# Optimization experiments

Measured on AMD Instinct MI355X. Metric: run time of the kernel, lower is better.

## Reference

```python
import jax, jax.numpy as jnp
import numpy as np

N = 100000      # nodes
E = 1600000     # edges
D = 128         # hidden_dim
H = 8           # num_heads
DH = D // H     # per-head dim (out_dim in MultiHeadAttentionLayer)
EPS = 1e-5


def layer_norm(x, g, b):
    mu = jnp.mean(x, axis=-1, keepdims=True)
    var = jnp.var(x, axis=-1, keepdims=True)
    return (x - mu) * jax.lax.rsqrt(var + EPS) * g + b


def setup_inputs() -> dict:
    key = jax.random.key(0)
    ks = jax.random.split(key, 16)
    s = 1.0 / np.sqrt(D)
    inp = {
        "h": jax.random.normal(ks[0], (N, D), jnp.float32),
        "src": jax.random.randint(ks[1], (E,), 0, N, jnp.int32),
        "dst": jax.random.randint(ks[2], (E,), 0, N, jnp.int32),
        # attention projections (use_bias=False)
        "Wq": jax.random.uniform(ks[3], (D, D), jnp.float32, -s, s),
        "Wk": jax.random.uniform(ks[4], (D, D), jnp.float32, -s, s),
        "Wv": jax.random.uniform(ks[5], (D, D), jnp.float32, -s, s),
        # output projection O (bias=True)
        "Wo": jax.random.uniform(ks[6], (D, D), jnp.float32, -s, s),
        "bo": jnp.zeros((D,), jnp.float32),
        # layer norms
        "g1": jnp.ones((D,), jnp.float32),
        "b1": jnp.zeros((D,), jnp.float32),
        "g2": jnp.ones((D,), jnp.float32),
        "b2": jnp.zeros((D,), jnp.float32),
        # FFN
        "W1": jax.random.uniform(ks[7], (D, 2 * D), jnp.float32, -s, s),
        "c1": jnp.zeros((2 * D,), jnp.float32),
        "W2": jax.random.uniform(ks[8], (2 * D, D), jnp.float32, -1.0 / np.sqrt(2 * D), 1.0 / np.sqrt(2 * D)),
        "c2": jnp.zeros((D,), jnp.float32),
    }
    return inp


def reference(h, src, dst, Wq, Wk, Wv, Wo, bo, g1, b1, g2, b2, W1, c1, W2, c2):
    n = h.shape[0]
    Q = (h @ Wq).reshape(n, H, DH)
    K = (h @ Wk).reshape(n, H, DH)
    V = (h @ Wv).reshape(n, H, DH)

    # per-edge score: (K[src] * Q[dst]).sum(-1), scaled exp with clamp
    score = jnp.einsum('ehd,ehd->eh', K[src], Q[dst])          # [E, H]
    score = jnp.exp(jnp.clip(score / np.sqrt(DH), -5.0, 5.0))  # [E, H]

    # scatter-sum aggregation into destination nodes
    wV = jax.ops.segment_sum(V[src] * score[:, :, None], dst, num_segments=n)  # [N, H, DH]
    z = jax.ops.segment_sum(score, dst, num_segments=n)                        # [N, H]

    # possible_empty=True: divide only where z > 0
    zb = z[:, :, None]
    head_out = jnp.where(zb > 0, wV / jnp.where(zb > 0, zb, 1.0), wV)

    a = head_out.reshape(n, D) @ Wo + bo
    hh = layer_norm(h + a, g1, b1)
    ff = jax.nn.relu(hh @ W1 + c1) @ W2 + c2
    return layer_norm(hh + ff, g2, b2)
```

## Files before the change

### kernel.cpp

```cpp
#include <hip/hip_runtime.h>
#include <hip/hip_bf16.h>

#define D 128

typedef __attribute__((ext_vector_type(8))) short short8;
typedef __attribute__((ext_vector_type(4))) float float4v;
typedef __attribute__((ext_vector_type(2))) float float2v;

__device__ __forceinline__ float4v mfma16(short8 a, short8 b, float4v c) {
  return __builtin_amdgcn_mfma_f32_16x16x32_bf16(a, b, c, 0, 0, 0);
}
__device__ __forceinline__ float b2f(__hip_bfloat16 x) { return __bfloat162float(x); }
__device__ __forceinline__ __hip_bfloat16 f2b(float x) { return __float2bfloat16(x); }
__device__ __forceinline__ unsigned short f2b_bits(float x) {
  __hip_bfloat16 h = __float2bfloat16(x);
  return *reinterpret_cast<unsigned short*>(&h);
}

__device__ __forceinline__ float ldf(const float* p, size_t i) { return p[i]; }
__device__ __forceinline__ float ldf(const __hip_bfloat16* p, size_t i) { return b2f(p[i]); }
__device__ __forceinline__ void stf(float* p, size_t i, float v) { p[i] = v; }
__device__ __forceinline__ void stf(__hip_bfloat16* p, size_t i, float v) { p[i] = f2b(v); }

__device__ __forceinline__ void unpack2(unsigned w, float& lo, float& hi) {
  lo = __uint_as_float(w << 16);
  hi = __uint_as_float(w & 0xffff0000u);
}
__device__ __forceinline__ float2v up2(unsigned w) {
  float2v r;
  r.x = __uint_as_float(w << 16);
  r.y = __uint_as_float(w & 0xffff0000u);
  return r;
}
__device__ __forceinline__ unsigned char f2fp8(float x) {
  int r = __builtin_amdgcn_cvt_pk_fp8_f32(x, x, 0, false);
  return (unsigned char)(r & 0xff);
}
__device__ __forceinline__ float2v cvt2lo(unsigned w) {
  return __builtin_amdgcn_cvt_pk_f32_fp8(w, false);
}
__device__ __forceinline__ float2v cvt2hi(unsigned w) {
  return __builtin_amdgcn_cvt_pk_f32_fp8(w, true);
}

__global__ void k_cast_w(const float* __restrict__ wq, const float* __restrict__ wk,
                         const float* __restrict__ wv, const float* __restrict__ wo,
                         const float* __restrict__ w1, const float* __restrict__ w2,
                         __hip_bfloat16* __restrict__ oq, __hip_bfloat16* __restrict__ ok,
                         __hip_bfloat16* __restrict__ ov, __hip_bfloat16* __restrict__ oo,
                         __hip_bfloat16* __restrict__ o1, __hip_bfloat16* __restrict__ o2) {
  int i = blockIdx.x * 256 + threadIdx.x;
  if (i < 49152) {
    int m = i & 16383;
    const float* s = (i < 16384) ? wq : (i < 32768) ? wk : wv;
    __hip_bfloat16* o = (i < 16384) ? oq : (i < 32768) ? ok : ov;
    int j = m & 7, t = m >> 3;
    int col = t & 127, cq = t >> 7;
    int row = (cq >> 2) * 32 + (cq & 3) * 8 + j;
    o[m] = f2b(s[row * 128 + col]);
  }
  else if (i < 65536) oo[i - 49152] = f2b(wo[i - 49152]);
  else if (i < 98304) o1[i - 65536] = f2b(w1[i - 65536]);
  else o2[i - 98304] = f2b(w2[i - 98304]);
}

#define MAXB 512

__global__ void k_bhist(const int* __restrict__ dst, int* __restrict__ bh, int E) {
  __shared__ int cnt[MAXB];
  for (int i = threadIdx.x; i < MAXB; i += 256) cnt[i] = 0;
  __syncthreads();
  for (int e = blockIdx.x * 256 + threadIdx.x; e < E; e += gridDim.x * 256)
    atomicAdd(&cnt[dst[e] >> 8], 1);
  __syncthreads();
  for (int i = threadIdx.x; i < MAXB; i += 256)
    if (cnt[i]) atomicAdd(&bh[i], cnt[i]);
}

__global__ void k_bscan(const int* __restrict__ bh, int* __restrict__ bbase,
                        int* __restrict__ bcur, int B) {
  __shared__ int sd[MAXB];
  int t = threadIdx.x;
  int v = (t < B) ? bh[t] : 0;
  sd[t] = v;
  __syncthreads();
  for (int o = 1; o < MAXB; o <<= 1) {
    int x = (t >= o) ? sd[t - o] : 0;
    __syncthreads();
    sd[t] += x;
    __syncthreads();
  }
  if (t < B) {
    int e = sd[t] - v;
    bbase[t] = e;
    bcur[t] = e;
  }
}

__global__ __launch_bounds__(256) void k_bin(const int* __restrict__ src,
                                             const int* __restrict__ dst,
                                             int* __restrict__ bcur,
                                             uint2* __restrict__ binned, int E) {
  __shared__ int cnt[MAXB];
  __shared__ int base[MAXB];
  const int t = threadIdx.x;
  const int e0 = blockIdx.x * 4096;
  for (int i = t; i < MAXB; i += 256) cnt[i] = 0;
  __syncthreads();
  int myb[16], myr[16], ms[16], md[16];
#pragma unroll
  for (int j = 0; j < 16; ++j) {
    int e = e0 + j * 256 + t;
    if (e < E) {
      int d = dst[e];
      ms[j] = src[e];
      md[j] = d;
      int b = d >> 8;
      myb[j] = b;
      myr[j] = atomicAdd(&cnt[b], 1);
    } else {
      myb[j] = -1;
    }
  }
  __syncthreads();
  for (int i = t; i < MAXB; i += 256)
    base[i] = cnt[i] ? atomicAdd(&bcur[i], cnt[i]) : 0;
  __syncthreads();
#pragma unroll
  for (int j = 0; j < 16; ++j)
    if (myb[j] >= 0)
      binned[(size_t)base[myb[j]] + myr[j]] = make_uint2((unsigned)ms[j], (unsigned)md[j]);
}

__global__ __launch_bounds__(256) void k_fine(const uint2* __restrict__ binned,
                                              const int* __restrict__ bh,
                                              const int* __restrict__ bbase,
                                              int* __restrict__ deg,
                                              int* __restrict__ offs,
                                              int* __restrict__ csr, int N) {
  __shared__ int cnt[256];
  __shared__ int cur[256];
  __shared__ int sd[256];
  const int b = blockIdx.x, t = threadIdx.x;
  const int node0 = b << 8;
  cnt[t] = 0;
  __syncthreads();
  const int s0 = bbase[b], len = bh[b];
  for (int i = t; i < len; i += 256) atomicAdd(&cnt[binned[(size_t)s0 + i].y & 255], 1);
  __syncthreads();
  int v = cnt[t];
  sd[t] = v;
  __syncthreads();
  for (int o = 1; o < 256; o <<= 1) {
    int x = (t >= o) ? sd[t - o] : 0;
    __syncthreads();
    sd[t] += x;
    __syncthreads();
  }
  int excl = sd[t] - v;
  cur[t] = excl;
  int node = node0 + t;
  if (node < N) {
    deg[node] = v;
    offs[node] = s0 + excl;
  }
  __syncthreads();
  for (int i = t; i < len; i += 256) {
    uint2 ed = binned[(size_t)s0 + i];
    int p = atomicAdd(&cur[ed.y & 255], 1);
    csr[s0 + p] = (int)ed.x;
  }
}

__global__ __launch_bounds__(512, 2) void gemm_qkv2(const float* __restrict__ A,
                                                    const short8* __restrict__ BqF,
                                                    const short8* __restrict__ BkF,
                                                    const short8* __restrict__ BvF,
                                                    __hip_bfloat16* __restrict__ Q,
                                                    unsigned char* __restrict__ KV8,
                                                    int Nrow) {
  const int t = threadIdx.x;
  const int lane = t & 63;
  const int ct = t >> 6;
  const int n = lane & 15, quad = lane >> 4;
  short8 fq[4], fk[4], fv[4];
#pragma unroll
  for (int c = 0; c < 4; ++c) {
    int fi = (c * 4 + quad) * 128 + ct * 16 + n;
    fq[c] = BqF[fi];
    fk[c] = BkF[fi];
    fv[c] = BvF[fi];
  }
  int ntiles = Nrow >> 4;
  const int koff = ct * 32 + ((n >> 3) << 4) + (n & 7);
  for (int rt = blockIdx.x; rt < ntiles; rt += gridDim.x) {
    float4v aq = {0.f, 0.f, 0.f, 0.f}, ak = aq, av = aq;
    const float* Ap = A + (size_t)(rt * 16 + n) * 128 + quad * 8;
#pragma unroll
    for (int c = 0; c < 4; ++c) {
      float4 u0 = *(const float4*)(Ap + c * 32);
      float4 u1 = *(const float4*)(Ap + c * 32 + 4);
      short8 a;
      a[0] = (short)f2b_bits(u0.x); a[1] = (short)f2b_bits(u0.y);
      a[2] = (short)f2b_bits(u0.z); a[3] = (short)f2b_bits(u0.w);
      a[4] = (short)f2b_bits(u1.x); a[5] = (short)f2b_bits(u1.y);
      a[6] = (short)f2b_bits(u1.z); a[7] = (short)f2b_bits(u1.w);
      aq = mfma16(a, fq[c], aq);
      ak = mfma16(a, fk[c], ak);
      av = mfma16(a, fv[c], av);
    }
#pragma unroll
    for (int r = 0; r < 4; ++r) {
      int grow = rt * 16 + quad * 4 + r;
      Q[(size_t)grow * 128 + ct * 16 + n] = f2b(aq[r]);
      size_t b = (size_t)grow * 256 + koff;
      KV8[b] = f2fp8(ak[r]);
      KV8[b + 8] = f2fp8(av[r]);
    }
  }
}

template <int K, typename TR, typename TO>
__global__ __launch_bounds__(512) void ln_gemm(const short* __restrict__ A,
                                               const short* __restrict__ B,
                                               const float* __restrict__ bias,
                                               const TR* __restrict__ resid,
                                               const float* __restrict__ gam,
                                               const float* __restrict__ bet,
                                               TO* __restrict__ Out, int Nrow) {
  __shared__ float tile[2][16][132];
  const int t = threadIdx.x;
  const int lane = t & 63;
  const int ct = t >> 6;
  const int n = lane & 15, quad = lane >> 4;
  short8 bfr[K / 32];
#pragma unroll
  for (int c = 0; c < K / 32; ++c) {
    short8 tmp;
#pragma unroll
    for (int j = 0; j < 8; ++j)
      tmp[j] = B[(size_t)(c * 32 + quad * 8 + j) * 128 + ct * 16 + n];
    bfr[c] = tmp;
  }
  float biasv = bias[ct * 16 + n];
  const int row2 = t >> 5, sub = t & 31;
  float ga0 = gam[sub],      ga1 = gam[sub + 32];
  float ga2 = gam[sub + 64], ga3 = gam[sub + 96];
  float be0 = bet[sub],      be1 = bet[sub + 32];
  float be2 = bet[sub + 64], be3 = bet[sub + 96];
  int ntiles = Nrow >> 4;
  int pp = 0;
  for (int rt = blockIdx.x; rt < ntiles; rt += gridDim.x, pp ^= 1) {
    float4v acc = {0.f, 0.f, 0.f, 0.f};
    const short* Ap = A + (size_t)(rt * 16 + n) * K + quad * 8;
#pragma unroll
    for (int c = 0; c < K / 32; ++c)
      acc = mfma16(*(const short8*)(Ap + c * 32), bfr[c], acc);
#pragma unroll
    for (int r = 0; r < 4; ++r) {
      int rr = quad * 4 + r;
      size_t g = (size_t)(rt * 16 + rr) * 128 + ct * 16 + n;
      tile[pp][rr][ct * 16 + n] = acc[r] + biasv + ldf(resid, g);
    }
    __syncthreads();
    float x0 = tile[pp][row2][sub], x1 = tile[pp][row2][sub + 32];
    float x2 = tile[pp][row2][sub + 64], x3 = tile[pp][row2][sub + 96];
    float s = x0 + x1 + x2 + x3;
    float s2 = x0 * x0 + x1 * x1 + x2 * x2 + x3 * x3;
#pragma unroll
    for (int o = 16; o >= 1; o >>= 1) {
      s += __shfl_xor(s, o);
      s2 += __shfl_xor(s2, o);
    }
    float mean = s * 0.0078125f;
    float var = s2 * 0.0078125f - mean * mean;
    float rstd = rsqrtf(var + 1e-5f);
    size_t base = (size_t)(rt * 16 + row2) * 128;
    stf(Out, base + sub,      (x0 - mean) * rstd * ga0 + be0);
    stf(Out, base + sub + 32, (x1 - mean) * rstd * ga1 + be1);
    stf(Out, base + sub + 64, (x2 - mean) * rstd * ga2 + be2);
    stf(Out, base + sub + 96, (x3 - mean) * rstd * ga3 + be3);
  }
}

__global__ __launch_bounds__(512) void ffn_ln(const short* __restrict__ hh,
                                              const short* __restrict__ W1b,
                                              const float* __restrict__ c1,
                                              const short* __restrict__ W2b,
                                              const float* __restrict__ c2,
                                              const float* __restrict__ gam,
                                              const float* __restrict__ bet,
                                              float* __restrict__ Out, int Nrow) {
  __shared__ short mid[16][264];
  __shared__ float tile[16][132];
  const int t = threadIdx.x;
  const int lane = t & 63;
  const int wv = t >> 6;
  const int n = lane & 15, quad = lane >> 4;
  short8 f1[2][4];
  float b1v[2];
#pragma unroll
  for (int cc = 0; cc < 2; ++cc) {
    int col = (wv * 2 + cc) * 16 + n;
#pragma unroll
    for (int c = 0; c < 4; ++c) {
      short8 tmp;
#pragma unroll
      for (int j = 0; j < 8; ++j)
        tmp[j] = W1b[(size_t)(c * 32 + quad * 8 + j) * 256 + col];
      f1[cc][c] = tmp;
    }
    b1v[cc] = c1[col];
  }
  short8 f2[8];
#pragma unroll
  for (int c = 0; c < 8; ++c) {
    short8 tmp;
#pragma unroll
    for (int j = 0; j < 8; ++j)
      tmp[j] = W2b[(size_t)(c * 32 + quad * 8 + j) * 128 + wv * 16 + n];
    f2[c] = tmp;
  }
  float b2v = c2[wv * 16 + n];
  const int row2 = t >> 5, sub = t & 31;
  float ga0 = gam[sub],      ga1 = gam[sub + 32];
  float ga2 = gam[sub + 64], ga3 = gam[sub + 96];
  float be0 = bet[sub],      be1 = bet[sub + 32];
  float be2 = bet[sub + 64], be3 = bet[sub + 96];
  int ntiles = Nrow >> 4;
  for (int rt = blockIdx.x; rt < ntiles; rt += gridDim.x) {
    float4v a1[2];
    a1[0] = (float4v){0.f, 0.f, 0.f, 0.f};
    a1[1] = a1[0];
    const short* Ap = hh + (size_t)(rt * 16 + n) * 128 + quad * 8;
#pragma unroll
    for (int c = 0; c < 4; ++c) {
      short8 a = *(const short8*)(Ap + c * 32);
      a1[0] = mfma16(a, f1[0][c], a1[0]);
      a1[1] = mfma16(a, f1[1][c], a1[1]);
    }
#pragma unroll
    for (int cc = 0; cc < 2; ++cc)
#pragma unroll
      for (int r = 0; r < 4; ++r)
        mid[quad * 4 + r][(wv * 2 + cc) * 16 + n] =
            (short)f2b_bits(fmaxf(a1[cc][r] + b1v[cc], 0.f));
    __syncthreads();
    float4v acc = {0.f, 0.f, 0.f, 0.f};
#pragma unroll
    for (int c = 0; c < 8; ++c) {
      short8 a = *(const short8*)&mid[n][quad * 8 + c * 32];
      acc = mfma16(a, f2[c], acc);
    }
#pragma unroll
    for (int r = 0; r < 4; ++r) {
      int rr = quad * 4 + r;
      size_t g = (size_t)(rt * 16 + rr) * 128 + wv * 16 + n;
      tile[rr][wv * 16 + n] = acc[r] + b2v + b2f(((const __hip_bfloat16*)hh)[g]);
    }
    __syncthreads();
    float x0 = tile[row2][sub], x1 = tile[row2][sub + 32];
    float x2 = tile[row2][sub + 64], x3 = tile[row2][sub + 96];
    float s = x0 + x1 + x2 + x3;
    float s2 = x0 * x0 + x1 * x1 + x2 * x2 + x3 * x3;
#pragma unroll
    for (int o = 16; o >= 1; o >>= 1) {
      s += __shfl_xor(s, o);
      s2 += __shfl_xor(s2, o);
    }
    float mean = s * 0.0078125f;
    float var = s2 * 0.0078125f - mean * mean;
    float rstd = rsqrtf(var + 1e-5f);
    size_t base = (size_t)(rt * 16 + row2) * 128;
    Out[base + sub]      = (x0 - mean) * rstd * ga0 + be0;
    Out[base + sub + 32] = (x1 - mean) * rstd * ga1 + be1;
    Out[base + sub + 64] = (x2 - mean) * rstd * ga2 + be2;
    Out[base + sub + 96] = (x3 - mean) * rstd * ga3 + be3;
  }
}

__global__ __launch_bounds__(256) void attn_agg5(const uint4* __restrict__ Q4,
                                                 const uint4* __restrict__ KV8,
                                                 const int* __restrict__ offs,
                                                 const int* __restrict__ deg,
                                                 const int* __restrict__ csr,
                                                 uint4* __restrict__ AT4, int N) {
  const int lane = threadIdx.x & 63;
  const int wv = threadIdx.x >> 6;
  const int e4 = lane >> 4;
  const int hd = (lane >> 1) & 7;
  const int hf = lane & 1;
  const int kvo = hd * 2 + hf;
  for (int node = blockIdx.x * 4 + wv; node < N; node += gridDim.x * 4) {
    uint4 qa = Q4[(size_t)node * 16 + kvo];
    float2v qv[4];
    qv[0] = up2(qa.x); qv[1] = up2(qa.y); qv[2] = up2(qa.z); qv[3] = up2(qa.w);
    float2v acc[4];
#pragma unroll
    for (int d = 0; d < 4; ++d) acc[d] = (float2v){0.f, 0.f};
    float z = 0.f;
    const int st = offs[node], dg = deg[node];
    if (dg > 0) {
      const int dgm1 = dg - 1;
      int s_cur = csr[st + min(e4, dgm1)];
      int s_nxt = (dg > 4) ? csr[st + min(4 + e4, dgm1)] : s_cur;
      uint4 ckv = KV8[(size_t)s_cur * 16 + kvo];
      int i = 0;
      while (true) {
        const bool more = (i + 4) < dg;
        uint4 nkv;
        int s_fut = s_nxt;
        if (more) {
          nkv = KV8[(size_t)s_nxt * 16 + kvo];
          s_fut = csr[st + min(i + 8 + e4, dgm1)];
        }
        float2v p2 = cvt2lo(ckv.x) * qv[0];
        p2 += cvt2hi(ckv.x) * qv[1];
        p2 += cvt2lo(ckv.y) * qv[2];
        p2 += cvt2hi(ckv.y) * qv[3];
        float p = p2.x + p2.y;
        p += __shfl_xor(p, 1);
        float sc = __expf(fminf(fmaxf(p * 0.25f, -5.f), 5.f));
        sc = ((i + e4) < dg) ? sc : 0.f;
        z += sc;
        float2v sv = {sc, sc};
        acc[0] += cvt2lo(ckv.z) * sv;
        acc[1] += cvt2hi(ckv.z) * sv;
        acc[2] += cvt2lo(ckv.w) * sv;
        acc[3] += cvt2hi(ckv.w) * sv;
        if (!more) break;
        ckv = nkv;
        s_nxt = s_fut;
        i += 4;
      }
    }
#pragma unroll
    for (int m = 16; m <= 32; m <<= 1) {
      z += __shfl_xor(z, m);
#pragma unroll
      for (int d = 0; d < 4; ++d) {
        acc[d].x += __shfl_xor(acc[d].x, m);
        acc[d].y += __shfl_xor(acc[d].y, m);
      }
    }
    if (e4 == 0) {
      float inv = (z > 0.f) ? 1.f / z : 1.f;
      unsigned r[4];
#pragma unroll
      for (int j = 0; j < 4; ++j)
        r[j] = (unsigned)f2b_bits(acc[j].x * inv) |
               ((unsigned)f2b_bits(acc[j].y * inv) << 16);
      AT4[(size_t)node * 16 + kvo] = make_uint4(r[0], r[1], r[2], r[3]);
    }
  }
}

extern "C" void kernel_launch(void* const* d_in, const int* in_sizes, int n_in,
                              void* d_out, int out_size, void* d_ws, size_t ws_size,
                              hipStream_t stream) {
  const float* h = (const float*)d_in[0];
  const int* src = (const int*)d_in[1];
  const int* dst = (const int*)d_in[2];
  const float* Wq = (const float*)d_in[3];
  const float* Wk = (const float*)d_in[4];
  const float* Wv = (const float*)d_in[5];
  const float* Wo = (const float*)d_in[6];
  const float* bo = (const float*)d_in[7];
  const float* g1 = (const float*)d_in[8];
  const float* b1 = (const float*)d_in[9];
  const float* g2 = (const float*)d_in[10];
  const float* b2 = (const float*)d_in[11];
  const float* W1 = (const float*)d_in[12];
  const float* c1 = (const float*)d_in[13];
  const float* W2 = (const float*)d_in[14];
  const float* c2 = (const float*)d_in[15];

  const int N = in_sizes[0] / D;
  const int E = in_sizes[1];
  const int B = (N + 255) >> 8;

  char* p = (char*)d_ws;
  auto carve = [&](size_t bytes) {
    char* r = p;
    p += (bytes + 255) & ~(size_t)255;
    return r;
  };
  short* ATb = (short*)carve((size_t)N * D * 2);
  short* Qb = (short*)carve((size_t)N * D * 2);
  unsigned char* KVb = (unsigned char*)carve((size_t)N * 256);
  short* wq = (short*)carve(16384 * 2);
  short* wk = (short*)carve(16384 * 2);
  short* wv = (short*)carve(16384 * 2);
  short* wo = (short*)carve(16384 * 2);
  short* w1 = (short*)carve(32768 * 2);
  short* w2 = (short*)carve(32768 * 2);
  int* deg = (int*)carve((size_t)N * 4);
  int* offs = (int*)carve((size_t)N * 4);
  int* bh = (int*)carve(MAXB * 4);
  int* bbase = (int*)carve(MAXB * 4);
  int* bcur = (int*)carve(MAXB * 4);
  uint2* binned = (uint2*)carve((size_t)E * 8);
  int* csr = (int*)carve((size_t)E * 4);
  short* hh = Qb;

  hipMemsetAsync(bh, 0, MAXB * 4, stream);
  k_bhist<<<1024, 256, 0, stream>>>(dst, bh, E);
  k_bscan<<<1, MAXB, 0, stream>>>(bh, bbase, bcur, B);
  k_bin<<<(E + 4095) / 4096, 256, 0, stream>>>(src, dst, bcur, binned, E);
  k_fine<<<B, 256, 0, stream>>>(binned, bh, bbase, deg, offs, csr, N);

  k_cast_w<<<512, 256, 0, stream>>>(Wq, Wk, Wv, Wo, W1, W2,
                                    (__hip_bfloat16*)wq, (__hip_bfloat16*)wk,
                                    (__hip_bfloat16*)wv, (__hip_bfloat16*)wo,
                                    (__hip_bfloat16*)w1, (__hip_bfloat16*)w2);

  gemm_qkv2<<<1536, 512, 0, stream>>>(h, (const short8*)wq, (const short8*)wk,
                                      (const short8*)wv, (__hip_bfloat16*)Qb, KVb, N);

  attn_agg5<<<(N + 3) >> 2, 256, 0, stream>>>((const uint4*)Qb, (const uint4*)KVb,
                                              offs, deg, csr, (uint4*)ATb, N);

  ln_gemm<128, float, __hip_bfloat16><<<1536, 512, 0, stream>>>(
      ATb, wo, bo, h, g1, b1, (__hip_bfloat16*)hh, N);
  ffn_ln<<<1536, 512, 0, stream>>>(hh, w1, c1, w2, c2, g2, b2, (float*)d_out, N);
}
```

Before: 408.5 us.

## Software-pipeline A-tile and residual loads across row tiles in GEMM kernels

The QKV, output-projection and FFN kernels now prefetch the next row tile's A operand and residual values into registers while the MFMA work and LayerNorm for the current tile run. This hides global load latency inside the persistent tile loops. Launch bounds are raised to ask for more waves per CU, and __syncthreads is replaced with a raw lgkmcnt wait plus s_barrier. The trade-off is higher register pressure, which can cause spills or cap occupancy, and the hand-written barrier waits only on LDS counters.

```diff
diff --git a/kernel.cpp b/kernel.cpp
--- a/kernel.cpp
+++ b/kernel.cpp
@@ -22,10 +22,10 @@
 __device__ __forceinline__ void stf(float* p, size_t i, float v) { p[i] = v; }
 __device__ __forceinline__ void stf(__hip_bfloat16* p, size_t i, float v) { p[i] = f2b(v); }
 
-__device__ __forceinline__ void unpack2(unsigned w, float& lo, float& hi) {
-  lo = __uint_as_float(w << 16);
-  hi = __uint_as_float(w & 0xffff0000u);
-}
+__device__ __forceinline__ void bar_lds() {
+  asm volatile("s_waitcnt lgkmcnt(0)\n\ts_barrier" ::: "memory");
+}
+
 __device__ __forceinline__ float2v up2(unsigned w) {
   float2v r;
   r.x = __uint_as_float(w << 16);
@@ -41,6 +41,15 @@
 }
 __device__ __forceinline__ float2v cvt2hi(unsigned w) {
   return __builtin_amdgcn_cvt_pk_f32_fp8(w, true);
+}
+
+__device__ __forceinline__ short8 cvt8(float4 u0, float4 u1) {
+  short8 a;
+  a[0] = (short)f2b_bits(u0.x); a[1] = (short)f2b_bits(u0.y);
+  a[2] = (short)f2b_bits(u0.z); a[3] = (short)f2b_bits(u0.w);
+  a[4] = (short)f2b_bits(u1.x); a[5] = (short)f2b_bits(u1.y);
+  a[6] = (short)f2b_bits(u1.z); a[7] = (short)f2b_bits(u1.w);
+  return a;
 }
 
 __global__ void k_cast_w(const float* __restrict__ wq, const float* __restrict__ wk,
@@ -172,7 +181,7 @@
   }
 }
 
-__global__ __launch_bounds__(512, 2) void gemm_qkv2(const float* __restrict__ A,
+__global__ __launch_bounds__(512, 4) void gemm_qkv3(const float* __restrict__ A,
                                                     const short8* __restrict__ BqF,
                                                     const short8* __restrict__ BkF,
                                                     const short8* __restrict__ BvF,
@@ -191,23 +200,38 @@
     fk[c] = BkF[fi];
     fv[c] = BvF[fi];
   }
-  int ntiles = Nrow >> 4;
+#pragma unroll
+  for (int c = 0; c < 4; ++c)
+    asm volatile("" : "+v"(fq[c]), "+v"(fk[c]), "+v"(fv[c]));
+  const int ntiles = Nrow >> 4;
   const int koff = ct * 32 + ((n >> 3) << 4) + (n & 7);
-  for (int rt = blockIdx.x; rt < ntiles; rt += gridDim.x) {
+  int rt = blockIdx.x;
+  if (rt >= ntiles) return;
+  short8 ab[4];
+  {
+    const float* Ap = A + (size_t)(rt * 16 + n) * 128 + quad * 8;
+#pragma unroll
+    for (int c = 0; c < 4; ++c)
+      ab[c] = cvt8(*(const float4*)(Ap + c * 32), *(const float4*)(Ap + c * 32 + 4));
+  }
+  while (true) {
+    const int rtn = rt + gridDim.x;
+    const bool more = rtn < ntiles;
+    float4 u2[8];
+    if (more) {
+      const float* Ap = A + (size_t)(rtn * 16 + n) * 128 + quad * 8;
+#pragma unroll
+      for (int c = 0; c < 4; ++c) {
+        u2[2 * c] = *(const float4*)(Ap + c * 32);
+        u2[2 * c + 1] = *(const float4*)(Ap + c * 32 + 4);
+      }
+    }
     float4v aq = {0.f, 0.f, 0.f, 0.f}, ak = aq, av = aq;
-    const float* Ap = A + (size_t)(rt * 16 + n) * 128 + quad * 8;
 #pragma unroll
     for (int c = 0; c < 4; ++c) {
-      float4 u0 = *(const float4*)(Ap + c * 32);
-      float4 u1 = *(const float4*)(Ap + c * 32 + 4);
-      short8 a;
-      a[0] = (short)f2b_bits(u0.x); a[1] = (short)f2b_bits(u0.y);
-      a[2] = (short)f2b_bits(u0.z); a[3] = (short)f2b_bits(u0.w);
-      a[4] = (short)f2b_bits(u1.x); a[5] = (short)f2b_bits(u1.y);
-      a[6] = (short)f2b_bits(u1.z); a[7] = (short)f2b_bits(u1.w);
-      aq = mfma16(a, fq[c], aq);
-      ak = mfma16(a, fk[c], ak);
-      av = mfma16(a, fv[c], av);
+      aq = mfma16(ab[c], fq[c], aq);
+      ak = mfma16(ab[c], fk[c], ak);
+      av = mfma16(ab[c], fv[c], av);
     }
 #pragma unroll
     for (int r = 0; r < 4; ++r) {
@@ -217,17 +241,21 @@
       KV8[b] = f2fp8(ak[r]);
       KV8[b + 8] = f2fp8(av[r]);
     }
+    if (!more) break;
+#pragma unroll
+    for (int c = 0; c < 4; ++c) ab[c] = cvt8(u2[2 * c], u2[2 * c + 1]);
+    rt = rtn;
   }
 }
 
 template <int K, typename TR, typename TO>
-__global__ __launch_bounds__(512) void ln_gemm(const short* __restrict__ A,
-                                               const short* __restrict__ B,
-                                               const float* __restrict__ bias,
-                                               const TR* __restrict__ resid,
-                                               const float* __restrict__ gam,
-                                               const float* __restrict__ bet,
-                                               TO* __restrict__ Out, int Nrow) {
+__global__ __launch_bounds__(512, 4) void ln_gemm(const short* __restrict__ A,
+                                                  const short* __restrict__ B,
+                                                  const float* __restrict__ bias,
+                                                  const TR* __restrict__ resid,
+                                                  const float* __restrict__ gam,
+                                                  const float* __restrict__ bet,
+                                                  TO* __restrict__ Out, int Nrow) {
   __shared__ float tile[2][16][132];
   const int t = threadIdx.x;
   const int lane = t & 63;
@@ -248,21 +276,40 @@
   float ga2 = gam[sub + 64], ga3 = gam[sub + 96];
   float be0 = bet[sub],      be1 = bet[sub + 32];
   float be2 = bet[sub + 64], be3 = bet[sub + 96];
-  int ntiles = Nrow >> 4;
+  const int ntiles = Nrow >> 4;
+  int rt = blockIdx.x;
+  if (rt >= ntiles) return;
+  short8 a[K / 32];
+  float rs[4];
+  {
+    const short* Ap = A + (size_t)(rt * 16 + n) * K + quad * 8;
+#pragma unroll
+    for (int c = 0; c < K / 32; ++c) a[c] = *(const short8*)(Ap + c * 32);
+#pragma unroll
+    for (int r = 0; r < 4; ++r)
+      rs[r] = ldf(resid, (size_t)(rt * 16 + quad * 4 + r) * 128 + ct * 16 + n);
+  }
   int pp = 0;
-  for (int rt = blockIdx.x; rt < ntiles; rt += gridDim.x, pp ^= 1) {
+  while (true) {
+    const int rtn = rt + gridDim.x;
+    const bool more = rtn < ntiles;
+    short8 an[K / 32];
+    float rsn[4];
+    if (more) {
+      const short* Ap = A + (size_t)(rtn * 16 + n) * K + quad * 8;
+#pragma unroll
+      for (int c = 0; c < K / 32; ++c) an[c] = *(const short8*)(Ap + c * 32);
+#pragma unroll
+      for (int r = 0; r < 4; ++r)
+        rsn[r] = ldf(resid, (size_t)(rtn * 16 + quad * 4 + r) * 128 + ct * 16 + n);
+    }
     float4v acc = {0.f, 0.f, 0.f, 0.f};
-    const short* Ap = A + (size_t)(rt * 16 + n) * K + quad * 8;
-#pragma unroll
-    for (int c = 0; c < K / 32; ++c)
-      acc = mfma16(*(const short8*)(Ap + c * 32), bfr[c], acc);
-#pragma unroll
-    for (int r = 0; r < 4; ++r) {
-      int rr = quad * 4 + r;
-      size_t g = (size_t)(rt * 16 + rr) * 128 + ct * 16 + n;
-      tile[pp][rr][ct * 16 + n] = acc[r] + biasv + ldf(resid, g);
-    }
-    __syncthreads();
+#pragma unroll
+    for (int c = 0; c < K / 32; ++c) acc = mfma16(a[c], bfr[c], acc);
+#pragma unroll
+    for (int r = 0; r < 4; ++r)
+      tile[pp][quad * 4 + r][ct * 16 + n] = acc[r] + biasv + rs[r];
+    bar_lds();
     float x0 = tile[pp][row2][sub], x1 = tile[pp][row2][sub + 32];
     float x2 = tile[pp][row2][sub + 64], x3 = tile[pp][row2][sub + 96];
     float s = x0 + x1 + x2 + x3;
@@ -280,17 +327,24 @@
     stf(Out, base + sub + 32, (x1 - mean) * rstd * ga1 + be1);
     stf(Out, base + sub + 64, (x2 - mean) * rstd * ga2 + be2);
     stf(Out, base + sub + 96, (x3 - mean) * rstd * ga3 + be3);
-  }
-}
-
-__global__ __launch_bounds__(512) void ffn_ln(const short* __restrict__ hh,
-                                              const short* __restrict__ W1b,
-                                              const float* __restrict__ c1,
-                                              const short* __restrict__ W2b,
-                                              const float* __restrict__ c2,
-                                              const float* __restrict__ gam,
-                                              const float* __restrict__ bet,
-                                              float* __restrict__ Out, int Nrow) {
+    if (!more) break;
+#pragma unroll
+    for (int c = 0; c < K / 32; ++c) a[c] = an[c];
+#pragma unroll
+    for (int r = 0; r < 4; ++r) rs[r] = rsn[r];
+    rt = rtn;
+    pp ^= 1;
+  }
+}
+
+__global__ __launch_bounds__(512, 2) void ffn_ln(const short* __restrict__ hh,
+                                                 const short* __restrict__ W1b,
+                                                 const float* __restrict__ c1,
+                                                 const short* __restrict__ W2b,
+                                                 const float* __restrict__ c2,
+                                                 const float* __restrict__ gam,
+                                                 const float* __restrict__ bet,
+                                                 float* __restrict__ Out, int Nrow) {
   __shared__ short mid[16][264];
   __shared__ float tile[16][132];
   const int t = threadIdx.x;
@@ -327,17 +381,40 @@
   float ga2 = gam[sub + 64], ga3 = gam[sub + 96];
   float be0 = bet[sub],      be1 = bet[sub + 32];
   float be2 = bet[sub + 64], be3 = bet[sub + 96];
-  int ntiles = Nrow >> 4;
-  for (int rt = blockIdx.x; rt < ntiles; rt += gridDim.x) {
+  const int ntiles = Nrow >> 4;
+  const __hip_bfloat16* hb = (const __hip_bfloat16*)hh;
+  int rt = blockIdx.x;
+  if (rt >= ntiles) return;
+  short8 a[4];
+  __hip_bfloat16 rs[4];
+  {
+    const short* Ap = hh + (size_t)(rt * 16 + n) * 128 + quad * 8;
+#pragma unroll
+    for (int c = 0; c < 4; ++c) a[c] = *(const short8*)(Ap + c * 32);
+#pragma unroll
+    for (int r = 0; r < 4; ++r)
+      rs[r] = hb[(size_t)(rt * 16 + quad * 4 + r) * 128 + wv * 16 + n];
+  }
+  while (true) {
+    const int rtn = rt + gridDim.x;
+    const bool more = rtn < ntiles;
+    short8 an[4];
+    __hip_bfloat16 rsn[4];
+    if (more) {
+      const short* Ap = hh + (size_t)(rtn * 16 + n) * 128 + quad * 8;
+#pragma unroll
+      for (int c = 0; c < 4; ++c) an[c] = *(const short8*)(Ap + c * 32);
+#pragma unroll
+      for (int r = 0; r < 4; ++r)
+        rsn[r] = hb[(size_t)(rtn * 16 + quad * 4 + r) * 128 + wv * 16 + n];
+    }
     float4v a1[2];
     a1[0] = (float4v){0.f, 0.f, 0.f, 0.f};
     a1[1] = a1[0];
-    const short* Ap = hh + (size_t)(rt * 16 + n) * 128 + quad * 8;
 #pragma unroll
     for (int c = 0; c < 4; ++c) {
-      short8 a = *(const short8*)(Ap + c * 32);
-      a1[0] = mfma16(a, f1[0][c], a1[0]);
-      a1[1] = mfma16(a, f1[1][c], a1[1]);
+      a1[0] = mfma16(a[c], f1[0][c], a1[0]);
+      a1[1] = mfma16(a[c], f1[1][c], a1[1]);
     }
 #pragma unroll
     for (int cc = 0; cc < 2; ++cc)
@@ -345,20 +422,17 @@
       for (int r = 0; r < 4; ++r)
         mid[quad * 4 + r][(wv * 2 + cc) * 16 + n] =
             (short)f2b_bits(fmaxf(a1[cc][r] + b1v[cc], 0.f));
-    __syncthreads();
+    bar_lds();
     float4v acc = {0.f, 0.f, 0.f, 0.f};
 #pragma unroll
     for (int c = 0; c < 8; ++c) {
-      short8 a = *(const short8*)&mid[n][quad * 8 + c * 32];
-      acc = mfma16(a, f2[c], acc);
-    }
-#pragma unroll
-    for (int r = 0; r < 4; ++r) {
-      int rr = quad * 4 + r;
-      size_t g = (size_t)(rt * 16 + rr) * 128 + wv * 16 + n;
-      tile[rr][wv * 16 + n] = acc[r] + b2v + b2f(((const __hip_bfloat16*)hh)[g]);
-    }
-    __syncthreads();
+      short8 am = *(const short8*)&mid[n][quad * 8 + c * 32];
+      acc = mfma16(am, f2[c], acc);
+    }
+#pragma unroll
+    for (int r = 0; r < 4; ++r)
+      tile[quad * 4 + r][wv * 16 + n] = acc[r] + b2v + b2f(rs[r]);
+    bar_lds();
     float x0 = tile[row2][sub], x1 = tile[row2][sub + 32];
     float x2 = tile[row2][sub + 64], x3 = tile[row2][sub + 96];
     float s = x0 + x1 + x2 + x3;
@@ -376,6 +450,12 @@
     Out[base + sub + 32] = (x1 - mean) * rstd * ga1 + be1;
     Out[base + sub + 64] = (x2 - mean) * rstd * ga2 + be2;
     Out[base + sub + 96] = (x3 - mean) * rstd * ga3 + be3;
+    if (!more) break;
+#pragma unroll
+    for (int c = 0; c < 4; ++c) a[c] = an[c];
+#pragma unroll
+    for (int r = 0; r < 4; ++r) rs[r] = rsn[r];
+    rt = rtn;
   }
 }
 
@@ -514,7 +594,7 @@
                                     (__hip_bfloat16*)wv, (__hip_bfloat16*)wo,
                                     (__hip_bfloat16*)w1, (__hip_bfloat16*)w2);
 
-  gemm_qkv2<<<1536, 512, 0, stream>>>(h, (const short8*)wq, (const short8*)wk,
+  gemm_qkv3<<<1536, 512, 0, stream>>>(h, (const short8*)wq, (const short8*)wk,
                                       (const short8*)wv, (__hip_bfloat16*)Qb, KVb, N);
 
   attn_agg5<<<(N + 3) >> 2, 256, 0, stream>>>((const uint4*)Qb, (const uint4*)KVb,
```

New measurement: 407.9 us. No clear change (-0.1%).

## Pre-swizzle all weights into MFMA fragment layout and reload per tile

Applied to the files above, without the earlier changes.

All GEMM weights, including Wo, W1 and W2, are now pre-arranged into MFMA B-fragment order in the cast kernel. Each GEMM loads its fragments as vector short8 reads inside the row-tile loop instead of keeping them in registers for the whole kernel. The gemm, LN-GEMM and FFN kernels also prefetch A and the residual values before the MFMAs, and replace __syncthreads with a custom lgkmcnt-wait barrier. This cuts register pressure and the strided scalar weight gathers, at the cost of re-reading weights from cache on every tile. An extra barrier is added at the end of the FFN loop to keep the LDS tile safe between iterations.

```diff
diff --git a/kernel.cpp b/kernel.cpp
--- a/kernel.cpp
+++ b/kernel.cpp
@@ -22,10 +22,10 @@
 __device__ __forceinline__ void stf(float* p, size_t i, float v) { p[i] = v; }
 __device__ __forceinline__ void stf(__hip_bfloat16* p, size_t i, float v) { p[i] = f2b(v); }
 
-__device__ __forceinline__ void unpack2(unsigned w, float& lo, float& hi) {
-  lo = __uint_as_float(w << 16);
-  hi = __uint_as_float(w & 0xffff0000u);
-}
+__device__ __forceinline__ void bar_lds() {
+  asm volatile("s_waitcnt lgkmcnt(0)\n\ts_barrier" ::: "memory");
+}
+
 __device__ __forceinline__ float2v up2(unsigned w) {
   float2v r;
   r.x = __uint_as_float(w << 16);
@@ -41,6 +41,15 @@
 }
 __device__ __forceinline__ float2v cvt2hi(unsigned w) {
   return __builtin_amdgcn_cvt_pk_f32_fp8(w, true);
+}
+
+__device__ __forceinline__ short8 cvt8(float4 u0, float4 u1) {
+  short8 a;
+  a[0] = (short)f2b_bits(u0.x); a[1] = (short)f2b_bits(u0.y);
+  a[2] = (short)f2b_bits(u0.z); a[3] = (short)f2b_bits(u0.w);
+  a[4] = (short)f2b_bits(u1.x); a[5] = (short)f2b_bits(u1.y);
+  a[6] = (short)f2b_bits(u1.z); a[7] = (short)f2b_bits(u1.w);
+  return a;
 }
 
 __global__ void k_cast_w(const float* __restrict__ wq, const float* __restrict__ wk,
@@ -50,18 +59,25 @@
                          __hip_bfloat16* __restrict__ ov, __hip_bfloat16* __restrict__ oo,
                          __hip_bfloat16* __restrict__ o1, __hip_bfloat16* __restrict__ o2) {
   int i = blockIdx.x * 256 + threadIdx.x;
-  if (i < 49152) {
+  if (i < 65536) {
     int m = i & 16383;
-    const float* s = (i < 16384) ? wq : (i < 32768) ? wk : wv;
-    __hip_bfloat16* o = (i < 16384) ? oq : (i < 32768) ? ok : ov;
-    int j = m & 7, t = m >> 3;
-    int col = t & 127, cq = t >> 7;
-    int row = (cq >> 2) * 32 + (cq & 3) * 8 + j;
-    o[m] = f2b(s[row * 128 + col]);
-  }
-  else if (i < 65536) oo[i - 49152] = f2b(wo[i - 49152]);
-  else if (i < 98304) o1[i - 65536] = f2b(w1[i - 65536]);
-  else o2[i - 98304] = f2b(w2[i - 98304]);
+    int which = i >> 14;
+    const float* s = (which == 0) ? wq : (which == 1) ? wk : (which == 2) ? wv : wo;
+    __hip_bfloat16* o = (which == 0) ? oq : (which == 1) ? ok : (which == 2) ? ov : oo;
+    int j = m & 7, t2 = m >> 3;
+    int col = t2 & 127, cq = t2 >> 7;
+    o[m] = f2b(s[((cq >> 2) * 32 + (cq & 3) * 8 + j) * 128 + col]);
+  } else if (i < 98304) {
+    int m = i - 65536;
+    int j = m & 7, t2 = m >> 3;
+    int col = t2 & 255, cq = t2 >> 8;
+    o1[m] = f2b(w1[((cq >> 2) * 32 + (cq & 3) * 8 + j) * 256 + col]);
+  } else {
+    int m = i - 98304;
+    int j = m & 7, t2 = m >> 3;
+    int col = t2 & 127, cq = t2 >> 7;
+    o2[m] = f2b(w2[((cq >> 2) * 32 + (cq & 3) * 8 + j) * 128 + col]);
+  }
 }
 
 #define MAXB 512
@@ -172,42 +188,40 @@
   }
 }
 
-__global__ __launch_bounds__(512, 2) void gemm_qkv2(const float* __restrict__ A,
-                                                    const short8* __restrict__ BqF,
-                                                    const short8* __restrict__ BkF,
-                                                    const short8* __restrict__ BvF,
-                                                    __hip_bfloat16* __restrict__ Q,
-                                                    unsigned char* __restrict__ KV8,
-                                                    int Nrow) {
+__global__ __launch_bounds__(512) void gemm_qkv4(const float* __restrict__ A,
+                                                 const short8* __restrict__ BqF,
+                                                 const short8* __restrict__ BkF,
+                                                 const short8* __restrict__ BvF,
+                                                 __hip_bfloat16* __restrict__ Q,
+                                                 unsigned char* __restrict__ KV8,
+                                                 int Nrow) {
   const int t = threadIdx.x;
   const int lane = t & 63;
   const int ct = t >> 6;
   const int n = lane & 15, quad = lane >> 4;
-  short8 fq[4], fk[4], fv[4];
-#pragma unroll
-  for (int c = 0; c < 4; ++c) {
-    int fi = (c * 4 + quad) * 128 + ct * 16 + n;
-    fq[c] = BqF[fi];
-    fk[c] = BkF[fi];
-    fv[c] = BvF[fi];
-  }
-  int ntiles = Nrow >> 4;
+  const short8* bq = BqF;
+  const short8* bk = BkF;
+  const short8* bv = BvF;
+  const int fbase = quad * 128 + ct * 16 + n;
+  const int ntiles = Nrow >> 4;
   const int koff = ct * 32 + ((n >> 3) << 4) + (n & 7);
   for (int rt = blockIdx.x; rt < ntiles; rt += gridDim.x) {
+    asm volatile("" : "+v"(bq), "+v"(bk), "+v"(bv));
+    const float* Ap = A + (size_t)(rt * 16 + n) * 128 + quad * 8;
+    short8 a[4], fq[4], fk[4], fv[4];
+#pragma unroll
+    for (int c = 0; c < 4; ++c) {
+      a[c] = cvt8(*(const float4*)(Ap + c * 32), *(const float4*)(Ap + c * 32 + 4));
+      fq[c] = bq[fbase + c * 512];
+      fk[c] = bk[fbase + c * 512];
+      fv[c] = bv[fbase + c * 512];
+    }
     float4v aq = {0.f, 0.f, 0.f, 0.f}, ak = aq, av = aq;
-    const float* Ap = A + (size_t)(rt * 16 + n) * 128 + quad * 8;
 #pragma unroll
     for (int c = 0; c < 4; ++c) {
-      float4 u0 = *(const float4*)(Ap + c * 32);
-      float4 u1 = *(const float4*)(Ap + c * 32 + 4);
-      short8 a;
-      a[0] = (short)f2b_bits(u0.x); a[1] = (short)f2b_bits(u0.y);
-      a[2] = (short)f2b_bits(u0.z); a[3] = (short)f2b_bits(u0.w);
-      a[4] = (short)f2b_bits(u1.x); a[5] = (short)f2b_bits(u1.y);
-      a[6] = (short)f2b_bits(u1.z); a[7] = (short)f2b_bits(u1.w);
-      aq = mfma16(a, fq[c], aq);
-      ak = mfma16(a, fk[c], ak);
-      av = mfma16(a, fv[c], av);
+      aq = mfma16(a[c], fq[c], aq);
+      ak = mfma16(a[c], fk[c], ak);
+      av = mfma16(a[c], fv[c], av);
     }
 #pragma unroll
     for (int r = 0; r < 4; ++r) {
@@ -222,7 +236,7 @@
 
 template <int K, typename TR, typename TO>
 __global__ __launch_bounds__(512) void ln_gemm(const short* __restrict__ A,
-                                               const short* __restrict__ B,
+                                               const short8* __restrict__ BF,
                                                const float* __restrict__ bias,
                                                const TR* __restrict__ resid,
                                                const float* __restrict__ gam,
@@ -233,36 +247,36 @@
   const int lane = t & 63;
   const int ct = t >> 6;
   const int n = lane & 15, quad = lane >> 4;
-  short8 bfr[K / 32];
-#pragma unroll
-  for (int c = 0; c < K / 32; ++c) {
-    short8 tmp;
-#pragma unroll
-    for (int j = 0; j < 8; ++j)
-      tmp[j] = B[(size_t)(c * 32 + quad * 8 + j) * 128 + ct * 16 + n];
-    bfr[c] = tmp;
-  }
+  const short8* bp = BF;
+  const int fbase = quad * 128 + ct * 16 + n;
   float biasv = bias[ct * 16 + n];
   const int row2 = t >> 5, sub = t & 31;
   float ga0 = gam[sub],      ga1 = gam[sub + 32];
   float ga2 = gam[sub + 64], ga3 = gam[sub + 96];
   float be0 = bet[sub],      be1 = bet[sub + 32];
   float be2 = bet[sub + 64], be3 = bet[sub + 96];
-  int ntiles = Nrow >> 4;
+  const int ntiles = Nrow >> 4;
   int pp = 0;
   for (int rt = blockIdx.x; rt < ntiles; rt += gridDim.x, pp ^= 1) {
+    asm volatile("" : "+v"(bp));
+    const short8* Ap = (const short8*)(A + (size_t)(rt * 16 + n) * K + quad * 8);
+    short8 a[K / 32], bf[K / 32];
+    float rs[4];
+#pragma unroll
+    for (int c = 0; c < K / 32; ++c) {
+      a[c] = Ap[c * 4];
+      bf[c] = bp[fbase + c * 512];
+    }
+#pragma unroll
+    for (int r = 0; r < 4; ++r)
+      rs[r] = ldf(resid, (size_t)(rt * 16 + quad * 4 + r) * 128 + ct * 16 + n);
     float4v acc = {0.f, 0.f, 0.f, 0.f};
-    const short* Ap = A + (size_t)(rt * 16 + n) * K + quad * 8;
-#pragma unroll
-    for (int c = 0; c < K / 32; ++c)
-      acc = mfma16(*(const short8*)(Ap + c * 32), bfr[c], acc);
-#pragma unroll
-    for (int r = 0; r < 4; ++r) {
-      int rr = quad * 4 + r;
-      size_t g = (size_t)(rt * 16 + rr) * 128 + ct * 16 + n;
-      tile[pp][rr][ct * 16 + n] = acc[r] + biasv + ldf(resid, g);
-    }
-    __syncthreads();
+#pragma unroll
+    for (int c = 0; c < K / 32; ++c) acc = mfma16(a[c], bf[c], acc);
+#pragma unroll
+    for (int r = 0; r < 4; ++r)
+      tile[pp][quad * 4 + r][ct * 16 + n] = acc[r] + biasv + rs[r];
+    bar_lds();
     float x0 = tile[pp][row2][sub], x1 = tile[pp][row2][sub + 32];
     float x2 = tile[pp][row2][sub + 64], x3 = tile[pp][row2][sub + 96];
     float s = x0 + x1 + x2 + x3;
@@ -284,9 +298,9 @@
 }
 
 __global__ __launch_bounds__(512) void ffn_ln(const short* __restrict__ hh,
-                                              const short* __restrict__ W1b,
+                                              const short8* __restrict__ W1F,
                                               const float* __restrict__ c1,
-                                              const short* __restrict__ W2b,
+                                              const short8* __restrict__ W2F,
                                               const float* __restrict__ c2,
                                               const float* __restrict__ gam,
                                               const float* __restrict__ bet,
@@ -297,68 +311,58 @@
   const int lane = t & 63;
   const int wv = t >> 6;
   const int n = lane & 15, quad = lane >> 4;
-  short8 f1[2][4];
-  float b1v[2];
-#pragma unroll
-  for (int cc = 0; cc < 2; ++cc) {
-    int col = (wv * 2 + cc) * 16 + n;
-#pragma unroll
-    for (int c = 0; c < 4; ++c) {
-      short8 tmp;
-#pragma unroll
-      for (int j = 0; j < 8; ++j)
-        tmp[j] = W1b[(size_t)(c * 32 + quad * 8 + j) * 256 + col];
-      f1[cc][c] = tmp;
-    }
-    b1v[cc] = c1[col];
-  }
-  short8 f2[8];
-#pragma unroll
-  for (int c = 0; c < 8; ++c) {
-    short8 tmp;
-#pragma unroll
-    for (int j = 0; j < 8; ++j)
-      tmp[j] = W2b[(size_t)(c * 32 + quad * 8 + j) * 128 + wv * 16 + n];
-    f2[c] = tmp;
-  }
+  const short8* p1 = W1F;
+  const short8* p2 = W2F;
+  float b1v0 = c1[(wv * 2) * 16 + n], b1v1 = c1[(wv * 2 + 1) * 16 + n];
   float b2v = c2[wv * 16 + n];
   const int row2 = t >> 5, sub = t & 31;
   float ga0 = gam[sub],      ga1 = gam[sub + 32];
   float ga2 = gam[sub + 64], ga3 = gam[sub + 96];
   float be0 = bet[sub],      be1 = bet[sub + 32];
   float be2 = bet[sub + 64], be3 = bet[sub + 96];
-  int ntiles = Nrow >> 4;
+  const int ntiles = Nrow >> 4;
+  const __hip_bfloat16* hb = (const __hip_bfloat16*)hh;
+  const int f1b0 = quad * 256 + (wv * 2) * 16 + n;
+  const int f1b1 = quad * 256 + (wv * 2 + 1) * 16 + n;
+  const int f2b = quad * 128 + wv * 16 + n;
   for (int rt = blockIdx.x; rt < ntiles; rt += gridDim.x) {
-    float4v a1[2];
-    a1[0] = (float4v){0.f, 0.f, 0.f, 0.f};
-    a1[1] = a1[0];
-    const short* Ap = hh + (size_t)(rt * 16 + n) * 128 + quad * 8;
+    asm volatile("" : "+v"(p1), "+v"(p2));
+    const short8* Ap = (const short8*)(hh + (size_t)(rt * 16 + n) * 128 + quad * 8);
+    short8 a[4], f1a[4], f1c[4], f2f[8];
+    __hip_bfloat16 rs[4];
 #pragma unroll
     for (int c = 0; c < 4; ++c) {
-      short8 a = *(const short8*)(Ap + c * 32);
-      a1[0] = mfma16(a, f1[0][c], a1[0]);
-      a1[1] = mfma16(a, f1[1][c], a1[1]);
-    }
-#pragma unroll
-    for (int cc = 0; cc < 2; ++cc)
-#pragma unroll
-      for (int r = 0; r < 4; ++r)
-        mid[quad * 4 + r][(wv * 2 + cc) * 16 + n] =
-            (short)f2b_bits(fmaxf(a1[cc][r] + b1v[cc], 0.f));
-    __syncthreads();
+      a[c] = Ap[c * 4];
+      f1a[c] = p1[f1b0 + c * 1024];
+      f1c[c] = p1[f1b1 + c * 1024];
+    }
+#pragma unroll
+    for (int c = 0; c < 8; ++c) f2f[c] = p2[f2b + c * 512];
+#pragma unroll
+    for (int r = 0; r < 4; ++r)
+      rs[r] = hb[(size_t)(rt * 16 + quad * 4 + r) * 128 + wv * 16 + n];
+    float4v a10 = {0.f, 0.f, 0.f, 0.f}, a11 = a10;
+#pragma unroll
+    for (int c = 0; c < 4; ++c) {
+      a10 = mfma16(a[c], f1a[c], a10);
+      a11 = mfma16(a[c], f1c[c], a11);
+    }
+#pragma unroll
+    for (int r = 0; r < 4; ++r) {
+      mid[quad * 4 + r][(wv * 2) * 16 + n] = (short)f2b_bits(fmaxf(a10[r] + b1v0, 0.f));
+      mid[quad * 4 + r][(wv * 2 + 1) * 16 + n] = (short)f2b_bits(fmaxf(a11[r] + b1v1, 0.f));
+    }
+    bar_lds();
     float4v acc = {0.f, 0.f, 0.f, 0.f};
 #pragma unroll
     for (int c = 0; c < 8; ++c) {
-      short8 a = *(const short8*)&mid[n][quad * 8 + c * 32];
-      acc = mfma16(a, f2[c], acc);
-    }
-#pragma unroll
-    for (int r = 0; r < 4; ++r) {
-      int rr = quad * 4 + r;
-      size_t g = (size_t)(rt * 16 + rr) * 128 + wv * 16 + n;
-      tile[rr][wv * 16 + n] = acc[r] + b2v + b2f(((const __hip_bfloat16*)hh)[g]);
-    }
-    __syncthreads();
+      short8 am = *(const short8*)&mid[n][quad * 8 + c * 32];
+      acc = mfma16(am, f2f[c], acc);
+    }
+#pragma unroll
+    for (int r = 0; r < 4; ++r)
+      tile[quad * 4 + r][wv * 16 + n] = acc[r] + b2v + b2f(rs[r]);
+    bar_lds();
     float x0 = tile[row2][sub], x1 = tile[row2][sub + 32];
     float x2 = tile[row2][sub + 64], x3 = tile[row2][sub + 96];
     float s = x0 + x1 + x2 + x3;
@@ -376,6 +380,7 @@
     Out[base + sub + 32] = (x1 - mean) * rstd * ga1 + be1;
     Out[base + sub + 64] = (x2 - mean) * rstd * ga2 + be2;
     Out[base + sub + 96] = (x3 - mean) * rstd * ga3 + be3;
+    bar_lds();
   }
 }
 
@@ -514,13 +519,14 @@
                                     (__hip_bfloat16*)wv, (__hip_bfloat16*)wo,
                                     (__hip_bfloat16*)w1, (__hip_bfloat16*)w2);
 
-  gemm_qkv2<<<1536, 512, 0, stream>>>(h, (const short8*)wq, (const short8*)wk,
+  gemm_qkv4<<<1536, 512, 0, stream>>>(h, (const short8*)wq, (const short8*)wk,
                                       (const short8*)wv, (__hip_bfloat16*)Qb, KVb, N);
 
   attn_agg5<<<(N + 3) >> 2, 256, 0, stream>>>((const uint4*)Qb, (const uint4*)KVb,
                                               offs, deg, csr, (uint4*)ATb, N);
 
   ln_gemm<128, float, __hip_bfloat16><<<1536, 512, 0, stream>>>(
-      ATb, wo, bo, h, g1, b1, (__hip_bfloat16*)hh, N);
-  ffn_ln<<<1536, 512, 0, stream>>>(hh, w1, c1, w2, c2, g2, b2, (float*)d_out, N);
-}
+      ATb, (const short8*)wo, bo, h, g1, b1, (__hip_bfloat16*)hh, N);
+  ffn_ln<<<1536, 512, 0, stream>>>(hh, (const short8*)w1, c1, (const short8*)w2, c2,
+                                   g2, b2, (float*)d_out, N);
+}
```

Measured after the change: 427.1 us. 4.6% more time.
